# Performance work log

Measured on AMD Instinct MI355X. Metric: run time of the kernel, lower is better.

## Reference

```python
import jax, jax.numpy as jnp
import numpy as np

N_NODES = 50000
N_EDGES = 800000
IN_F = 128
HID_F = 128
OUT_F = 128

def safediv(a, b):
    b = jnp.where(b == 0, jnp.ones_like(b), b)
    return a / b

def setup_inputs() -> dict:
    key = jax.random.key(0)
    ks = jax.random.split(key, 8)
    h = jax.random.normal(ks[0], (N_NODES, IN_F), dtype=jnp.float32)
    ppr_weight = jax.random.uniform(ks[1], (N_EDGES,), dtype=jnp.float32)
    Qw = jax.random.normal(ks[2], (HID_F, IN_F), dtype=jnp.float32) * (1.0 / np.sqrt(IN_F))
    Qb = jnp.zeros((HID_F,), dtype=jnp.float32)
    Ww = jax.random.normal(ks[3], (OUT_F, IN_F + HID_F), dtype=jnp.float32) * (1.0 / np.sqrt(IN_F + HID_F))
    Wb = jnp.zeros((OUT_F,), dtype=jnp.float32)
    src = jax.random.randint(ks[4], (N_EDGES,), 0, N_NODES, dtype=jnp.int64 if jax.config.jax_enable_x64 else jnp.int32)
    dst = jax.random.randint(ks[5], (N_EDGES,), 0, N_NODES, dtype=jnp.int64 if jax.config.jax_enable_x64 else jnp.int32)
    return {"h": h, "ppr_weight": ppr_weight, "Qw": Qw, "Qb": Qb, "Ww": Ww, "Wb": Wb, "src": src, "dst": dst}

def reference(h, ppr_weight, Qw, Qb, Ww, Wb, src, dst):
    # neighbor transform: Q(h) -> [N, HID_F]
    hq = h @ Qw.T + Qb
    # message: h_w = hq[src] * ppr_weight  (edge-weighted gather) [E, HID_F]
    msg = hq[src] * ppr_weight[:, None]
    # reduce: scatter-sum messages and weights onto dst nodes
    h_agg = jax.ops.segment_sum(msg, dst, num_segments=N_NODES)
    w = jax.ops.segment_sum(ppr_weight, dst, num_segments=N_NODES)
    # apply: PPR-weighted mean, concat, linear, leaky_relu, L2 normalize
    h_agg = safediv(h_agg, w[:, None])
    h_concat = jnp.concatenate([h, h_agg], axis=1)
    h_new = jax.nn.leaky_relu(h_concat @ Ww.T + Wb, negative_slope=0.01)
    norm = jnp.linalg.norm(h_new, axis=1, keepdims=True)
    return safediv(h_new, norm)
```

## Files before the change

kernel.cpp:

```cpp
#include <hip/hip_runtime.h>
#include <stdint.h>

#define N_NODES 50000
#define N_EDGES 800000
#define IN_F 128
#define HID_F 128
#define OUT_F 128
#define CAT_F 256
#define N_STRIPS 3125

#define NB 256
#define CHUNK 3136
#define NBUCK 3125
#define BCAP 384

typedef __bf16 bf16x8 __attribute__((ext_vector_type(8)));
typedef float f32x4 __attribute__((ext_vector_type(4)));

__device__ __forceinline__ uint32_t f2b(float f) {
  uint32_t u = __float_as_uint(f);
  return (u + 0x7fffu + ((u >> 16) & 1u)) >> 16;
}

__global__ void __launch_bounds__(256) prep_hist_kernel(
    const int* __restrict__ dst, int* __restrict__ G, const float* __restrict__ h,
    const float* __restrict__ Qw, const float* __restrict__ Ww, uint16_t* __restrict__ hB,
    uint16_t* __restrict__ QwB, uint16_t* __restrict__ WwB) {
  if (blockIdx.x < NB) {
    __shared__ int hist[NBUCK];
    for (int k = threadIdx.x; k < NBUCK; k += 256) hist[k] = 0;
    __syncthreads();
    int b = blockIdx.x;
    int base = b * CHUNK;
    int end = (base + CHUNK < N_EDGES) ? (base + CHUNK) : N_EDGES;
    for (int i4 = base / 4 + threadIdx.x; i4 * 4 < end; i4 += 256) {
      int4 d4 = ((const int4*)dst)[i4];
      atomicAdd(&hist[d4.x >> 4], 1);
      atomicAdd(&hist[d4.y >> 4], 1);
      atomicAdd(&hist[d4.z >> 4], 1);
      atomicAdd(&hist[d4.w >> 4], 1);
    }
    __syncthreads();
    for (int k = threadIdx.x; k < NBUCK; k += 256) G[k * NB + b] = hist[k];
  } else {
    const int TOT4 = (N_NODES * IN_F + HID_F * IN_F + OUT_F * CAT_F) / 4;
    int i4 = (blockIdx.x - NB) * 256 + threadIdx.x;
    if (i4 >= TOT4) return;
    int base = i4 * 4;
    const float* src;
    uint16_t* dstp;
    int off;
    if (base < N_NODES * IN_F) {
      src = h; dstp = hB; off = base;
    } else if (base < N_NODES * IN_F + HID_F * IN_F) {
      src = Qw; dstp = QwB; off = base - N_NODES * IN_F;
    } else {
      src = Ww; dstp = WwB; off = base - N_NODES * IN_F - HID_F * IN_F;
    }
    float4 v = *(const float4*)(src + off);
    ushort4 o;
    o.x = (uint16_t)f2b(v.x); o.y = (uint16_t)f2b(v.y);
    o.z = (uint16_t)f2b(v.z); o.w = (uint16_t)f2b(v.w);
    *(ushort4*)(dstp + off) = o;
  }
}

__global__ void __launch_bounds__(256) bucket_scan_kernel(const int* __restrict__ G,
                                                          int* __restrict__ Gs,
                                                          int* __restrict__ Btot) {
  int w = (blockIdx.x * 256 + (int)threadIdx.x) >> 6;
  if (w >= NBUCK) return;
  int lane = threadIdx.x & 63;
  int4 v = *(const int4*)(G + (size_t)w * NB + lane * 4);
  int s = v.x + v.y + v.z + v.w;
  int inc = s;
#pragma unroll
  for (int d = 1; d < 64; d <<= 1) {
    int x = __shfl_up(inc, d, 64);
    if (lane >= d) inc += x;
  }
  int exc = inc - s;
  int4 o;
  o.x = exc;
  o.y = exc + v.x;
  o.z = exc + v.x + v.y;
  o.w = exc + v.x + v.y + v.z;
  *(int4*)(Gs + (size_t)w * NB + lane * 4) = o;
  if (lane == 63) Btot[w] = inc;
}

__global__ void base_scan_kernel(const int* __restrict__ Btot, int* __restrict__ Bbase) {
  int lane = threadIdx.x;
  int c[49], loc[49];
  int s = 0;
#pragma unroll
  for (int j = 0; j < 49; ++j) {
    int i = lane * 49 + j;
    c[j] = (i < NBUCK) ? Btot[i] : 0;
    loc[j] = s;
    s += c[j];
  }
  int inc = s;
#pragma unroll
  for (int d = 1; d < 64; d <<= 1) {
    int x = __shfl_up(inc, d, 64);
    if (lane >= d) inc += x;
  }
  int exc = inc - s;
#pragma unroll
  for (int j = 0; j < 49; ++j) {
    int i = lane * 49 + j;
    if (i <= NBUCK) Bbase[i] = exc + loc[j];
  }
}

__device__ __forceinline__ void gemm1_body(int gb, const uint16_t* __restrict__ hB,
                                           const uint16_t* __restrict__ QwB,
                                           const float* __restrict__ Qb,
                                           uint16_t* __restrict__ hqB) {
  int wave = (gb * 256 + (int)threadIdx.x) >> 6;
  if (wave >= N_STRIPS) return;
  int lane = threadIdx.x & 63;
  int r = lane & 15, qd = lane >> 4;
  int row0 = wave * 16;
  f32x4 acc[8];
#pragma unroll
  for (int t = 0; t < 8; ++t) acc[t] = (f32x4){0.f, 0.f, 0.f, 0.f};
  const uint16_t* aRow = hB + (size_t)(row0 + r) * IN_F + qd * 8;
#pragma unroll
  for (int kt = 0; kt < 4; ++kt) {
    bf16x8 a = *(const bf16x8*)(aRow + kt * 32);
#pragma unroll
    for (int t = 0; t < 8; ++t) {
      bf16x8 b = *(const bf16x8*)(QwB + (t * 16 + r) * IN_F + kt * 32 + qd * 8);
      acc[t] = __builtin_amdgcn_mfma_f32_16x16x32_bf16(a, b, acc[t], 0, 0, 0);
    }
  }
#pragma unroll
  for (int t = 0; t < 8; ++t) {
    float qb = Qb[t * 16 + r];
#pragma unroll
    for (int rr = 0; rr < 4; ++rr) {
      int m = row0 + qd * 4 + rr;
      hqB[(size_t)m * HID_F + t * 16 + r] = (uint16_t)f2b(acc[t][rr] + qb);
    }
  }
}

__global__ void __launch_bounds__(256) scatter_gemm1_kernel(
    const int* __restrict__ dst, const int* __restrict__ src, const float* __restrict__ ppr,
    const int* __restrict__ Gs, const int* __restrict__ Bbase, int2* __restrict__ rec,
    const uint16_t* __restrict__ hB, const uint16_t* __restrict__ QwB,
    const float* __restrict__ Qb, uint16_t* __restrict__ hqB) {
  if (blockIdx.x < NB) {
    __shared__ int cursor[NBUCK];
    int b = blockIdx.x;
    for (int k = threadIdx.x; k < NBUCK; k += 256)
      cursor[k] = Bbase[k] + Gs[(size_t)k * NB + b];
    __syncthreads();
    int base = b * CHUNK;
    int end = (base + CHUNK < N_EDGES) ? (base + CHUNK) : N_EDGES;
    for (int i4 = base / 4 + threadIdx.x; i4 * 4 < end; i4 += 256) {
      int4 d4 = ((const int4*)dst)[i4];
      int4 s4 = ((const int4*)src)[i4];
      float4 w4 = ((const float4*)ppr)[i4];
      int p;
      p = atomicAdd(&cursor[d4.x >> 4], 1);
      rec[p] = make_int2(s4.x | ((d4.x & 15) << 20), __float_as_int(w4.x));
      p = atomicAdd(&cursor[d4.y >> 4], 1);
      rec[p] = make_int2(s4.y | ((d4.y & 15) << 20), __float_as_int(w4.y));
      p = atomicAdd(&cursor[d4.z >> 4], 1);
      rec[p] = make_int2(s4.z | ((d4.z & 15) << 20), __float_as_int(w4.z));
      p = atomicAdd(&cursor[d4.w >> 4], 1);
      rec[p] = make_int2(s4.w | ((d4.w & 15) << 20), __float_as_int(w4.w));
    }
  } else {
    gemm1_body(blockIdx.x - NB, hB, QwB, Qb, hqB);
  }
}

__global__ void __launch_bounds__(256) agg_gemm2_kernel(
    const uint16_t* __restrict__ hqB, const int2* __restrict__ rec,
    const int* __restrict__ Bbase, const uint16_t* __restrict__ hB,
    const uint16_t* __restrict__ WwB, const float* __restrict__ Wb,
    float* __restrict__ out) {
  __shared__ int2 srec[BCAP];
  __shared__ uint4 hagg[16][17];
  __shared__ int hist[16];
  __shared__ int noff[17];
  __shared__ int cur[16];
  int g = blockIdx.x;
  int t = threadIdx.x;
  if (t < 16) hist[t] = 0;
  __syncthreads();

  int rbeg = Bbase[g];
  int len = Bbase[g + 1] - rbeg;
  len = (len < BCAP) ? len : BCAP;

  int2 rc[2];
#pragma unroll
  for (int k = 0; k < 2; ++k) {
    int i = t + k * 256;
    if (i < len) {
      rc[k] = rec[rbeg + i];
      atomicAdd(&hist[rc[k].x >> 20], 1);
    }
  }
  __syncthreads();

  if (t < 16) {
    int v = hist[t];
    int inc = v;
#pragma unroll
    for (int d = 1; d < 16; d <<= 1) {
      int x = __shfl_up(inc, d, 64);
      if (t >= d) inc += x;
    }
    noff[t] = inc - v;
    cur[t] = inc - v;
    if (t == 15) noff[16] = inc;
  }
  __syncthreads();

#pragma unroll
  for (int k = 0; k < 2; ++k) {
    int i = t + k * 256;
    if (i < len) {
      int p = atomicAdd(&cur[rc[k].x >> 20], 1);
      srec[p] = rc[k];
    }
  }
  __syncthreads();

  {
    int gs = t >> 4, c = t & 15;
    const uint4* hq4 = (const uint4*)hqB;
    int nl = gs;
    int nbeg = noff[nl], nend = noff[nl + 1];
    int last = nend - 1;
    float a[8];
#pragma unroll
    for (int j = 0; j < 8; ++j) a[j] = 0.f;
    float ws = 0.f;

    int2 rrA[4], rrB[4];
    uint4 uA[4], uB[4];

#define LOADB(E0, RR, UU)                                         \
  {                                                               \
    _Pragma("unroll") for (int j = 0; j < 4; ++j) {               \
      int i = (E0) + j;                                           \
      RR[j] = srec[(i < last) ? i : last];                        \
    }                                                             \
    _Pragma("unroll") for (int j = 0; j < 4; ++j)                 \
        UU[j] = hq4[(size_t)(RR[j].x & 0xFFFFF) * 16 + c];        \
  }

#define CONSB(E0, RR, UU)                                           \
  {                                                                 \
    _Pragma("unroll") for (int j = 0; j < 4; ++j) {                 \
      float w = ((E0) + j < nend) ? __int_as_float(RR[j].y) : 0.f;  \
      ws += w;                                                      \
      uint32_t x;                                                   \
      x = UU[j].x;                                                  \
      a[0] += w * __uint_as_float(x << 16);                         \
      a[1] += w * __uint_as_float(x & 0xffff0000u);                 \
      x = UU[j].y;                                                  \
      a[2] += w * __uint_as_float(x << 16);                         \
      a[3] += w * __uint_as_float(x & 0xffff0000u);                 \
      x = UU[j].z;                                                  \
      a[4] += w * __uint_as_float(x << 16);                         \
      a[5] += w * __uint_as_float(x & 0xffff0000u);                 \
      x = UU[j].w;                                                  \
      a[6] += w * __uint_as_float(x << 16);                         \
      a[7] += w * __uint_as_float(x & 0xffff0000u);                 \
    }                                                               \
  }

    int e = nbeg;
    if (e < nend) {
      LOADB(e, rrA, uA);
      while (true) {
        int eB = e + 4;
        if (eB < nend) {
          LOADB(eB, rrB, uB);
          CONSB(e, rrA, uA);
          int eA = eB + 4;
          if (eA < nend) {
            LOADB(eA, rrA, uA);
            CONSB(eB, rrB, uB);
            e = eA;
          } else {
            CONSB(eB, rrB, uB);
            break;
          }
        } else {
          CONSB(e, rrA, uA);
          break;
        }
      }
    }
#undef LOADB
#undef CONSB

    float dnm = (ws == 0.f) ? 1.f : ws;
    float inv = 1.f / dnm;
    uint4 o;
    o.x = f2b(a[0] * inv) | (f2b(a[1] * inv) << 16);
    o.y = f2b(a[2] * inv) | (f2b(a[3] * inv) << 16);
    o.z = f2b(a[4] * inv) | (f2b(a[5] * inv) << 16);
    o.w = f2b(a[6] * inv) | (f2b(a[7] * inv) << 16);
    hagg[nl][c] = o;
  }
  __syncthreads();

  int lane = t & 63, wv = t >> 6;
  if (wv != 0) return;
  int row0 = g * 16;
  int r = lane & 15, qd = lane >> 4;
  f32x4 acc[8];
#pragma unroll
  for (int tt = 0; tt < 8; ++tt) acc[tt] = (f32x4){0.f, 0.f, 0.f, 0.f};
  const uint16_t* aRow = hB + (size_t)(row0 + r) * IN_F + qd * 8;
#pragma unroll
  for (int kt = 0; kt < 8; ++kt) {
    bf16x8 av;
    if (kt < 4) {
      av = *(const bf16x8*)(aRow + kt * 32);
    } else {
      av = *(const bf16x8*)&hagg[r][(kt - 4) * 4 + qd];
    }
#pragma unroll
    for (int tt = 0; tt < 8; ++tt) {
      bf16x8 b = *(const bf16x8*)(WwB + (tt * 16 + r) * CAT_F + kt * 32 + qd * 8);
      acc[tt] = __builtin_amdgcn_mfma_f32_16x16x32_bf16(av, b, acc[tt], 0, 0, 0);
    }
  }
  float lv[8][4];
  float ss[4] = {0.f, 0.f, 0.f, 0.f};
#pragma unroll
  for (int tt = 0; tt < 8; ++tt) {
    float wb = Wb[tt * 16 + r];
#pragma unroll
    for (int rr2 = 0; rr2 < 4; ++rr2) {
      float v = acc[tt][rr2] + wb;
      v = (v >= 0.f) ? v : 0.01f * v;
      lv[tt][rr2] = v;
      ss[rr2] += v * v;
    }
  }
#pragma unroll
  for (int rr2 = 0; rr2 < 4; ++rr2) {
    float s = ss[rr2];
    s += __shfl_xor(s, 1);
    s += __shfl_xor(s, 2);
    s += __shfl_xor(s, 4);
    s += __shfl_xor(s, 8);
    float nr = sqrtf(s);
    float inv = (nr == 0.f) ? 1.f : (1.f / nr);
    int mrow = row0 + qd * 4 + rr2;
    float* orow = out + (size_t)mrow * OUT_F;
#pragma unroll
    for (int tt = 0; tt < 8; ++tt) orow[tt * 16 + r] = lv[tt][rr2] * inv;
  }
}

extern "C" void kernel_launch(void* const* d_in, const int* in_sizes, int n_in,
                              void* d_out, int out_size, void* d_ws, size_t ws_size,
                              hipStream_t stream) {
  const float* h = (const float*)d_in[0];
  const float* ppr = (const float*)d_in[1];
  const float* Qw = (const float*)d_in[2];
  const float* Qb = (const float*)d_in[3];
  const float* Ww = (const float*)d_in[4];
  const float* Wb = (const float*)d_in[5];
  const int* src = (const int*)d_in[6];
  const int* dst = (const int*)d_in[7];
  float* out = (float*)d_out;

  char* ws = (char*)d_ws;
  size_t o = 0;
  auto alloc = [&](size_t bytes) {
    void* p = ws + o;
    o = (o + bytes + 255) & ~(size_t)255;
    return p;
  };
  uint16_t* hB = (uint16_t*)alloc((size_t)N_NODES * IN_F * 2);
  uint16_t* hqB = (uint16_t*)alloc((size_t)N_NODES * HID_F * 2);
  uint16_t* QwB = (uint16_t*)alloc((size_t)HID_F * IN_F * 2);
  uint16_t* WwB = (uint16_t*)alloc((size_t)OUT_F * CAT_F * 2);
  int* G = (int*)alloc((size_t)NBUCK * NB * 4);
  int* Gs = (int*)alloc((size_t)NBUCK * NB * 4);
  int* Btot = (int*)alloc((size_t)NBUCK * 4);
  int* Bbase = (int*)alloc((size_t)(NBUCK + 1) * 4);
  int2* rec = (int2*)alloc((size_t)N_EDGES * 8);

  const int CONV_BLOCKS = ((N_NODES * IN_F + HID_F * IN_F + OUT_F * CAT_F) / 4 + 255) / 256;
  prep_hist_kernel<<<NB + CONV_BLOCKS, 256, 0, stream>>>(dst, G, h, Qw, Ww, hB, QwB, WwB);
  bucket_scan_kernel<<<(NBUCK + 3) / 4, 256, 0, stream>>>(G, Gs, Btot);
  base_scan_kernel<<<1, 64, 0, stream>>>(Btot, Bbase);
  scatter_gemm1_kernel<<<NB + 782, 256, 0, stream>>>(dst, src, ppr, Gs, Bbase, rec, hB, QwB,
                                                     Qb, hqB);
  agg_gemm2_kernel<<<NBUCK, 256, 0, stream>>>(hqB, rec, Bbase, hB, WwB, Wb, out);
}
```

Before: 180.8 us.

## Aggregate raw features before Q transform and replace per-block histograms with global atomics

Uses linearity to gather and average bf16 h rows per destination and then apply Qw to the 16-row aggregate inside the final kernel. This removes the separate hq GEMM and its intermediate buffer, and the bias is masked for zero-weight nodes. Bucket counting and scatter now use global atomics on a single cursor array instead of per-block shared histograms and a two-level scan, which cuts two kernels and the large G/Gs arrays. The final GEMM is split across all four waves, with a shared-memory reduction for the row norm. The trade-off is heavy global atomic contention, and the record order within buckets becomes nondeterministic.

After: 307.5 us. 1.7x slower.

```diff
diff --git a/kernel.cpp b/kernel.cpp
--- a/kernel.cpp
+++ b/kernel.cpp
@@ -7,12 +7,11 @@
 #define HID_F 128
 #define OUT_F 128
 #define CAT_F 256
-#define N_STRIPS 3125
-
-#define NB 256
-#define CHUNK 3136
+
 #define NBUCK 3125
 #define BCAP 384
+#define HB 392
+#define NI4 (N_EDGES / 4)
 
 typedef __bf16 bf16x8 __attribute__((ext_vector_type(8)));
 typedef float f32x4 __attribute__((ext_vector_type(4)));
@@ -22,29 +21,22 @@
   return (u + 0x7fffu + ((u >> 16) & 1u)) >> 16;
 }
 
-__global__ void __launch_bounds__(256) prep_hist_kernel(
-    const int* __restrict__ dst, int* __restrict__ G, const float* __restrict__ h,
+__global__ void __launch_bounds__(256) prep_kernel(
+    const int* __restrict__ dst, int* __restrict__ gcur, const float* __restrict__ h,
     const float* __restrict__ Qw, const float* __restrict__ Ww, uint16_t* __restrict__ hB,
     uint16_t* __restrict__ QwB, uint16_t* __restrict__ WwB) {
-  if (blockIdx.x < NB) {
-    __shared__ int hist[NBUCK];
-    for (int k = threadIdx.x; k < NBUCK; k += 256) hist[k] = 0;
-    __syncthreads();
-    int b = blockIdx.x;
-    int base = b * CHUNK;
-    int end = (base + CHUNK < N_EDGES) ? (base + CHUNK) : N_EDGES;
-    for (int i4 = base / 4 + threadIdx.x; i4 * 4 < end; i4 += 256) {
+  if (blockIdx.x < HB) {
+    int tid = blockIdx.x * 256 + threadIdx.x;
+    for (int i4 = tid; i4 < NI4; i4 += HB * 256) {
       int4 d4 = ((const int4*)dst)[i4];
-      atomicAdd(&hist[d4.x >> 4], 1);
-      atomicAdd(&hist[d4.y >> 4], 1);
-      atomicAdd(&hist[d4.z >> 4], 1);
-      atomicAdd(&hist[d4.w >> 4], 1);
-    }
-    __syncthreads();
-    for (int k = threadIdx.x; k < NBUCK; k += 256) G[k * NB + b] = hist[k];
+      atomicAdd(&gcur[d4.x >> 4], 1);
+      atomicAdd(&gcur[d4.y >> 4], 1);
+      atomicAdd(&gcur[d4.z >> 4], 1);
+      atomicAdd(&gcur[d4.w >> 4], 1);
+    }
   } else {
     const int TOT4 = (N_NODES * IN_F + HID_F * IN_F + OUT_F * CAT_F) / 4;
-    int i4 = (blockIdx.x - NB) * 256 + threadIdx.x;
+    int i4 = (blockIdx.x - HB) * 256 + threadIdx.x;
     if (i4 >= TOT4) return;
     int base = i4 * 4;
     const float* src;
@@ -65,14 +57,17 @@
   }
 }
 
-__global__ void __launch_bounds__(256) bucket_scan_kernel(const int* __restrict__ G,
-                                                          int* __restrict__ Gs,
-                                                          int* __restrict__ Btot) {
-  int w = (blockIdx.x * 256 + (int)threadIdx.x) >> 6;
-  if (w >= NBUCK) return;
-  int lane = threadIdx.x & 63;
-  int4 v = *(const int4*)(G + (size_t)w * NB + lane * 4);
-  int s = v.x + v.y + v.z + v.w;
+__global__ void scan_kernel(int* __restrict__ gcur, int* __restrict__ Bbase) {
+  int lane = threadIdx.x;
+  int c[49], loc[49];
+  int s = 0;
+#pragma unroll
+  for (int j = 0; j < 49; ++j) {
+    int i = lane * 49 + j;
+    c[j] = (i < NBUCK) ? gcur[i] : 0;
+    loc[j] = s;
+    s += c[j];
+  }
   int inc = s;
 #pragma unroll
   for (int d = 1; d < 64; d <<= 1) {
@@ -80,115 +75,47 @@
     if (lane >= d) inc += x;
   }
   int exc = inc - s;
-  int4 o;
-  o.x = exc;
-  o.y = exc + v.x;
-  o.z = exc + v.x + v.y;
-  o.w = exc + v.x + v.y + v.z;
-  *(int4*)(Gs + (size_t)w * NB + lane * 4) = o;
-  if (lane == 63) Btot[w] = inc;
-}
-
-__global__ void base_scan_kernel(const int* __restrict__ Btot, int* __restrict__ Bbase) {
-  int lane = threadIdx.x;
-  int c[49], loc[49];
-  int s = 0;
 #pragma unroll
   for (int j = 0; j < 49; ++j) {
     int i = lane * 49 + j;
-    c[j] = (i < NBUCK) ? Btot[i] : 0;
-    loc[j] = s;
-    s += c[j];
-  }
-  int inc = s;
-#pragma unroll
-  for (int d = 1; d < 64; d <<= 1) {
-    int x = __shfl_up(inc, d, 64);
-    if (lane >= d) inc += x;
-  }
-  int exc = inc - s;
-#pragma unroll
-  for (int j = 0; j < 49; ++j) {
-    int i = lane * 49 + j;
-    if (i <= NBUCK) Bbase[i] = exc + loc[j];
-  }
-}
-
-__device__ __forceinline__ void gemm1_body(int gb, const uint16_t* __restrict__ hB,
-                                           const uint16_t* __restrict__ QwB,
-                                           const float* __restrict__ Qb,
-                                           uint16_t* __restrict__ hqB) {
-  int wave = (gb * 256 + (int)threadIdx.x) >> 6;
-  if (wave >= N_STRIPS) return;
-  int lane = threadIdx.x & 63;
-  int r = lane & 15, qd = lane >> 4;
-  int row0 = wave * 16;
-  f32x4 acc[8];
-#pragma unroll
-  for (int t = 0; t < 8; ++t) acc[t] = (f32x4){0.f, 0.f, 0.f, 0.f};
-  const uint16_t* aRow = hB + (size_t)(row0 + r) * IN_F + qd * 8;
-#pragma unroll
-  for (int kt = 0; kt < 4; ++kt) {
-    bf16x8 a = *(const bf16x8*)(aRow + kt * 32);
-#pragma unroll
-    for (int t = 0; t < 8; ++t) {
-      bf16x8 b = *(const bf16x8*)(QwB + (t * 16 + r) * IN_F + kt * 32 + qd * 8);
-      acc[t] = __builtin_amdgcn_mfma_f32_16x16x32_bf16(a, b, acc[t], 0, 0, 0);
-    }
-  }
-#pragma unroll
-  for (int t = 0; t < 8; ++t) {
-    float qb = Qb[t * 16 + r];
-#pragma unroll
-    for (int rr = 0; rr < 4; ++rr) {
-      int m = row0 + qd * 4 + rr;
-      hqB[(size_t)m * HID_F + t * 16 + r] = (uint16_t)f2b(acc[t][rr] + qb);
-    }
-  }
-}
-
-__global__ void __launch_bounds__(256) scatter_gemm1_kernel(
+    int v = exc + loc[j];
+    if (i <= NBUCK) Bbase[i] = v;
+    if (i < NBUCK) gcur[i] = v;
+  }
+}
+
+__global__ void __launch_bounds__(256) scatter_kernel(
     const int* __restrict__ dst, const int* __restrict__ src, const float* __restrict__ ppr,
-    const int* __restrict__ Gs, const int* __restrict__ Bbase, int2* __restrict__ rec,
+    int* __restrict__ gcur, int2* __restrict__ rec) {
+  int i4 = blockIdx.x * 256 + threadIdx.x;
+  if (i4 >= NI4) return;
+  int4 d4 = ((const int4*)dst)[i4];
+  int4 s4 = ((const int4*)src)[i4];
+  float4 w4 = ((const float4*)ppr)[i4];
+  int p;
+  p = atomicAdd(&gcur[d4.x >> 4], 1);
+  rec[p] = make_int2(s4.x | ((d4.x & 15) << 20), __float_as_int(w4.x));
+  p = atomicAdd(&gcur[d4.y >> 4], 1);
+  rec[p] = make_int2(s4.y | ((d4.y & 15) << 20), __float_as_int(w4.y));
+  p = atomicAdd(&gcur[d4.z >> 4], 1);
+  rec[p] = make_int2(s4.z | ((d4.z & 15) << 20), __float_as_int(w4.z));
+  p = atomicAdd(&gcur[d4.w >> 4], 1);
+  rec[p] = make_int2(s4.w | ((d4.w & 15) << 20), __float_as_int(w4.w));
+}
+
+__global__ void __launch_bounds__(256) agg_gemm2_kernel(
+    const int2* __restrict__ rec, const int* __restrict__ Bbase,
     const uint16_t* __restrict__ hB, const uint16_t* __restrict__ QwB,
-    const float* __restrict__ Qb, uint16_t* __restrict__ hqB) {
-  if (blockIdx.x < NB) {
-    __shared__ int cursor[NBUCK];
-    int b = blockIdx.x;
-    for (int k = threadIdx.x; k < NBUCK; k += 256)
-      cursor[k] = Bbase[k] + Gs[(size_t)k * NB + b];
-    __syncthreads();
-    int base = b * CHUNK;
-    int end = (base + CHUNK < N_EDGES) ? (base + CHUNK) : N_EDGES;
-    for (int i4 = base / 4 + threadIdx.x; i4 * 4 < end; i4 += 256) {
-      int4 d4 = ((const int4*)dst)[i4];
-      int4 s4 = ((const int4*)src)[i4];
-      float4 w4 = ((const float4*)ppr)[i4];
-      int p;
-      p = atomicAdd(&cursor[d4.x >> 4], 1);
-      rec[p] = make_int2(s4.x | ((d4.x & 15) << 20), __float_as_int(w4.x));
-      p = atomicAdd(&cursor[d4.y >> 4], 1);
-      rec[p] = make_int2(s4.y | ((d4.y & 15) << 20), __float_as_int(w4.y));
-      p = atomicAdd(&cursor[d4.z >> 4], 1);
-      rec[p] = make_int2(s4.z | ((d4.z & 15) << 20), __float_as_int(w4.z));
-      p = atomicAdd(&cursor[d4.w >> 4], 1);
-      rec[p] = make_int2(s4.w | ((d4.w & 15) << 20), __float_as_int(w4.w));
-    }
-  } else {
-    gemm1_body(blockIdx.x - NB, hB, QwB, Qb, hqB);
-  }
-}
-
-__global__ void __launch_bounds__(256) agg_gemm2_kernel(
-    const uint16_t* __restrict__ hqB, const int2* __restrict__ rec,
-    const int* __restrict__ Bbase, const uint16_t* __restrict__ hB,
-    const uint16_t* __restrict__ WwB, const float* __restrict__ Wb,
-    float* __restrict__ out) {
+    const float* __restrict__ Qb, const uint16_t* __restrict__ WwB,
+    const float* __restrict__ Wb, float* __restrict__ out) {
   __shared__ int2 srec[BCAP];
   __shared__ uint4 hagg[16][17];
+  __shared__ uint4 hq2[16][17];
   __shared__ int hist[16];
   __shared__ int noff[17];
   __shared__ int cur[16];
+  __shared__ float wsum[16];
+  __shared__ float ssp[4][16];
   int g = blockIdx.x;
   int t = threadIdx.x;
   if (t < 16) hist[t] = 0;
@@ -235,7 +162,7 @@
 
   {
     int gs = t >> 4, c = t & 15;
-    const uint4* hq4 = (const uint4*)hqB;
+    const uint4* hb4 = (const uint4*)hB;
     int nl = gs;
     int nbeg = noff[nl], nend = noff[nl + 1];
     int last = nend - 1;
@@ -254,7 +181,7 @@
       RR[j] = srec[(i < last) ? i : last];                        \
     }                                                             \
     _Pragma("unroll") for (int j = 0; j < 4; ++j)                 \
-        UU[j] = hq4[(size_t)(RR[j].x & 0xFFFFF) * 16 + c];        \
+        UU[j] = hb4[(size_t)(RR[j].x & 0xFFFFF) * 16 + c];        \
   }
 
 #define CONSB(E0, RR, UU)                                           \
@@ -312,16 +239,37 @@
     o.z = f2b(a[4] * inv) | (f2b(a[5] * inv) << 16);
     o.w = f2b(a[6] * inv) | (f2b(a[7] * inv) << 16);
     hagg[nl][c] = o;
+    if (c == 0) wsum[nl] = ws;
   }
   __syncthreads();
 
   int lane = t & 63, wv = t >> 6;
-  if (wv != 0) return;
+  int r = lane & 15, qd = lane >> 4;
+
+#pragma unroll
+  for (int tq = 0; tq < 2; ++tq) {
+    int tt = wv * 2 + tq;
+    f32x4 acc = (f32x4){0.f, 0.f, 0.f, 0.f};
+#pragma unroll
+    for (int kt = 0; kt < 4; ++kt) {
+      bf16x8 av = *(const bf16x8*)&hagg[r][kt * 4 + qd];
+      bf16x8 b = *(const bf16x8*)(QwB + (tt * 16 + r) * IN_F + kt * 32 + qd * 8);
+      acc = __builtin_amdgcn_mfma_f32_16x16x32_bf16(av, b, acc, 0, 0, 0);
+    }
+    float qb = Qb[tt * 16 + r];
+#pragma unroll
+    for (int rr2 = 0; rr2 < 4; ++rr2) {
+      int row = qd * 4 + rr2;
+      float flag = (wsum[row] != 0.f) ? 1.f : 0.f;
+      ((uint16_t*)&hq2[row][0])[tt * 16 + r] = (uint16_t)f2b(acc[rr2] + qb * flag);
+    }
+  }
+  __syncthreads();
+
   int row0 = g * 16;
-  int r = lane & 15, qd = lane >> 4;
-  f32x4 acc[8];
-#pragma unroll
-  for (int tt = 0; tt < 8; ++tt) acc[tt] = (f32x4){0.f, 0.f, 0.f, 0.f};
+  f32x4 acc2[2];
+  acc2[0] = (f32x4){0.f, 0.f, 0.f, 0.f};
+  acc2[1] = (f32x4){0.f, 0.f, 0.f, 0.f};
   const uint16_t* aRow = hB + (size_t)(row0 + r) * IN_F + qd * 8;
 #pragma unroll
   for (int kt = 0; kt < 8; ++kt) {
@@ -329,24 +277,26 @@
     if (kt < 4) {
       av = *(const bf16x8*)(aRow + kt * 32);
     } else {
-      av = *(const bf16x8*)&hagg[r][(kt - 4) * 4 + qd];
-    }
-#pragma unroll
-    for (int tt = 0; tt < 8; ++tt) {
+      av = *(const bf16x8*)&hq2[r][(kt - 4) * 4 + qd];
+    }
+#pragma unroll
+    for (int tq = 0; tq < 2; ++tq) {
+      int tt = wv * 2 + tq;
       bf16x8 b = *(const bf16x8*)(WwB + (tt * 16 + r) * CAT_F + kt * 32 + qd * 8);
-      acc[tt] = __builtin_amdgcn_mfma_f32_16x16x32_bf16(av, b, acc[tt], 0, 0, 0);
-    }
-  }
-  float lv[8][4];
+      acc2[tq] = __builtin_amdgcn_mfma_f32_16x16x32_bf16(av, b, acc2[tq], 0, 0, 0);
+    }
+  }
+  float lv[2][4];
   float ss[4] = {0.f, 0.f, 0.f, 0.f};
 #pragma unroll
-  for (int tt = 0; tt < 8; ++tt) {
+  for (int tq = 0; tq < 2; ++tq) {
+    int tt = wv * 2 + tq;
     float wb = Wb[tt * 16 + r];
 #pragma unroll
     for (int rr2 = 0; rr2 < 4; ++rr2) {
-      float v = acc[tt][rr2] + wb;
+      float v = acc2[tq][rr2] + wb;
       v = (v >= 0.f) ? v : 0.01f * v;
-      lv[tt][rr2] = v;
+      lv[tq][rr2] = v;
       ss[rr2] += v * v;
     }
   }
@@ -357,12 +307,25 @@
     s += __shfl_xor(s, 2);
     s += __shfl_xor(s, 4);
     s += __shfl_xor(s, 8);
-    float nr = sqrtf(s);
+    ss[rr2] = s;
+  }
+  if (r == 0) {
+#pragma unroll
+    for (int rr2 = 0; rr2 < 4; ++rr2) ssp[wv][qd * 4 + rr2] = ss[rr2];
+  }
+  __syncthreads();
+#pragma unroll
+  for (int rr2 = 0; rr2 < 4; ++rr2) {
+    int row = qd * 4 + rr2;
+    float tot = ssp[0][row] + ssp[1][row] + ssp[2][row] + ssp[3][row];
+    float nr = sqrtf(tot);
     float inv = (nr == 0.f) ? 1.f : (1.f / nr);
-    int mrow = row0 + qd * 4 + rr2;
-    float* orow = out + (size_t)mrow * OUT_F;
-#pragma unroll
-    for (int tt = 0; tt < 8; ++tt) orow[tt * 16 + r] = lv[tt][rr2] * inv;
+    float* orow = out + (size_t)(row0 + row) * OUT_F;
+#pragma unroll
+    for (int tq = 0; tq < 2; ++tq) {
+      int tt = wv * 2 + tq;
+      orow[tt * 16 + r] = lv[tq][rr2] * inv;
+    }
   }
 }
 
@@ -387,20 +350,16 @@
     return p;
   };
   uint16_t* hB = (uint16_t*)alloc((size_t)N_NODES * IN_F * 2);
-  uint16_t* hqB = (uint16_t*)alloc((size_t)N_NODES * HID_F * 2);
   uint16_t* QwB = (uint16_t*)alloc((size_t)HID_F * IN_F * 2);
   uint16_t* WwB = (uint16_t*)alloc((size_t)OUT_F * CAT_F * 2);
-  int* G = (int*)alloc((size_t)NBUCK * NB * 4);
-  int* Gs = (int*)alloc((size_t)NBUCK * NB * 4);
-  int* Btot = (int*)alloc((size_t)NBUCK * 4);
+  int* gcur = (int*)alloc((size_t)NBUCK * 4);
   int* Bbase = (int*)alloc((size_t)(NBUCK + 1) * 4);
   int2* rec = (int2*)alloc((size_t)N_EDGES * 8);
 
   const int CONV_BLOCKS = ((N_NODES * IN_F + HID_F * IN_F + OUT_F * CAT_F) / 4 + 255) / 256;
-  prep_hist_kernel<<<NB + CONV_BLOCKS, 256, 0, stream>>>(dst, G, h, Qw, Ww, hB, QwB, WwB);
-  bucket_scan_kernel<<<(NBUCK + 3) / 4, 256, 0, stream>>>(G, Gs, Btot);
-  base_scan_kernel<<<1, 64, 0, stream>>>(Btot, Bbase);
-  scatter_gemm1_kernel<<<NB + 782, 256, 0, stream>>>(dst, src, ppr, Gs, Bbase, rec, hB, QwB,
-                                                     Qb, hqB);
-  agg_gemm2_kernel<<<NBUCK, 256, 0, stream>>>(hqB, rec, Bbase, hB, WwB, Wb, out);
-}
+  hipMemsetAsync(gcur, 0, (size_t)NBUCK * 4, stream);
+  prep_kernel<<<HB + CONV_BLOCKS, 256, 0, stream>>>(dst, gcur, h, Qw, Ww, hB, QwB, WwB);
+  scan_kernel<<<1, 64, 0, stream>>>(gcur, Bbase);
+  scatter_kernel<<<(NI4 + 255) / 256, 256, 0, stream>>>(dst, src, ppr, gcur, rec);
+  agg_gemm2_kernel<<<NBUCK, 256, 0, stream>>>(rec, Bbase, hB, QwB, Qb, WwB, Wb, out);
+}
```
